# Kernel tuning notes

Hardware: AMD Instinct MI355X
Metric: run time of the kernel (lower is better)

Reference implementation:

```python
import jax, jax.numpy as jnp
import numpy as np

B, L, D, H, DH, MAX_SEQ = 2, 2048, 512, 8, 64, 2048


def setup_inputs() -> dict:
    key = jax.random.key(0)
    ks = jax.random.split(key, 9)
    w = 0.02
    return {
        "q": jax.random.normal(ks[0], (B, L, D), jnp.float32),
        "k": jax.random.normal(ks[1], (B, L, D), jnp.float32),
        "v": jax.random.normal(ks[2], (B, L, D), jnp.float32),
        "Wq_w": jax.random.normal(ks[3], (D, D), jnp.float32) * w,
        "Wq_b": jnp.zeros((D,), jnp.float32),
        "Wk_w": jax.random.normal(ks[4], (D, D), jnp.float32) * w,
        "Wk_b": jnp.zeros((D,), jnp.float32),
        "Wv_w": jax.random.normal(ks[5], (D, D), jnp.float32) * w,
        "Wv_b": jnp.zeros((D,), jnp.float32),
        "fc_w": jax.random.normal(ks[6], (D, D), jnp.float32) * w,
        "fc_b": jnp.zeros((D,), jnp.float32),
        "E": jax.random.normal(ks[7], (MAX_SEQ, DH), jnp.float32),
        "mask": jnp.triu(jnp.ones((L, L), jnp.int32), k=1)[None, None],  # 1 = masked
    }


def reference(q, k, v, Wq_w, Wq_b, Wk_w, Wk_b, Wv_w, Wv_b, fc_w, fc_b, E, mask):
    b, lq, d = q.shape

    def proj(x, w, bias):
        # torch Linear: x @ W.T + b, then split heads -> [b, h, l, dh]
        y = x @ w.T + bias
        return y.reshape(b, -1, H, DH).transpose(0, 2, 1, 3)

    qh, kh, vh = proj(q, Wq_w, Wq_b), proj(k, Wk_w, Wk_b), proj(v, Wv_w, Wv_b)
    len_q, len_k = qh.shape[2], kh.shape[2]

    # relative embedding slice (starting_point = max(0, max_seq - len_q))
    e = E[max(0, MAX_SEQ - len_q):, :]          # [m, dh], m == len_q here
    m = e.shape[0]

    QE = jnp.einsum('bhld,md->bhlm', qh, e)      # [b,h,lq,m]
    # qe_masking: keep column j of row i iff j >= m-1-i
    keep = (jnp.arange(m)[None, :] >= (m - 1 - jnp.arange(len_q))[:, None])
    QE = QE * keep.astype(QE.dtype)

    # skewing: left-pad last dim, reshape swapping trailing dims, drop first row
    padded = jnp.pad(QE, ((0, 0), (0, 0), (0, 0), (1, 0)))      # [b,h,lq,m+1]
    Srel = padded.reshape(b, H, m + 1, len_q)[:, :, 1:, :]       # [b,h,m,lq]
    if len_k > len_q:
        Srel = jnp.pad(Srel, ((0, 0), (0, 0), (0, len_k - len_q), (0, 0)))
    elif len_k < len_q:
        Srel = Srel[:, :, :, :len_k]

    QKt = jnp.einsum('bhld,bhmd->bhlm', qh, kh)                  # [b,h,lq,lk]
    logits = (QKt + Srel) / jnp.sqrt(jnp.float32(DH))
    logits = logits + mask.astype(logits.dtype) * jnp.float32(-1e9)
    attn = jax.nn.softmax(logits, axis=-1)
    out = jnp.einsum('bhlm,bhmd->bhld', attn, vh)                # [b,h,lq,dh]
    out = out.transpose(0, 2, 1, 3).reshape(b, len_q, d)
    out = out @ fc_w.T + fc_b
    return out, attn
```

## Files before the change

### kernel.cpp

```cpp
#include <hip/hip_runtime.h>
#include <hip/hip_bf16.h>
#include <cstdint>

typedef __bf16 bf16;
typedef __attribute__((ext_vector_type(8))) __bf16 bf16x8;
typedef __attribute__((ext_vector_type(4))) __bf16 bf16x4;
typedef __attribute__((ext_vector_type(4))) float f32x4;

#define MFMA16 __builtin_amdgcn_mfma_f32_16x16x32_bf16
#define MASKV (-1e30f)

static constexpr int Lq  = 2048;
static constexpr int BQ  = 64;
static constexpr int BKt = 64;
static constexpr int TW  = 84;

__device__ __forceinline__ void async_load16(const void* g, void* l) {
  __builtin_amdgcn_global_load_lds(
      (__attribute__((address_space(1))) void*)g,
      (__attribute__((address_space(3))) void*)l, 16, 0, 0);
}

__global__ void convert_all(const float* __restrict__ q, const float* __restrict__ k,
                            const float* __restrict__ v, const float* __restrict__ wq,
                            const float* __restrict__ wk, const float* __restrict__ wv,
                            const float* __restrict__ fc, const float* __restrict__ E,
                            bf16* q_bf, bf16* k_bf, bf16* v_bf, bf16* wq_bf,
                            bf16* wk_bf, bf16* wv_bf, bf16* fc_bf, bf16* E_bf)
{
  int i = blockIdx.x * blockDim.x + threadIdx.x;
  const float* src; bf16* dst; int rel;
  if      (i < 524288)  { src = q;  dst = q_bf;  rel = i; }
  else if (i < 1048576) { src = k;  dst = k_bf;  rel = i - 524288; }
  else if (i < 1572864) { src = v;  dst = v_bf;  rel = i - 1048576; }
  else if (i < 1638400) { src = wq; dst = wq_bf; rel = i - 1572864; }
  else if (i < 1703936) { src = wk; dst = wk_bf; rel = i - 1638400; }
  else if (i < 1769472) { src = wv; dst = wv_bf; rel = i - 1703936; }
  else if (i < 1835008) { src = fc; dst = fc_bf; rel = i - 1769472; }
  else if (i < 1867776) { src = E;  dst = E_bf;  rel = i - 1835008; }
  else return;
  float4 x = *(const float4*)(src + (size_t)rel * 4);
  bf16x4 o;
  o[0] = (bf16)x.x; o[1] = (bf16)x.y; o[2] = (bf16)x.z; o[3] = (bf16)x.w;
  *(bf16x4*)(dst + (size_t)rel * 4) = o;
}

__global__ void zero_s(float* __restrict__ s_buf) {
  int i = blockIdx.x * blockDim.x + threadIdx.x;
  if (i < 8192) ((float4*)s_buf)[i] = make_float4(0.f, 0.f, 0.f, 0.f);
}

__global__ void combine_o(const bf16* __restrict__ O0, const bf16* __restrict__ O1,
                          bf16* __restrict__ oh) {
  int i = blockIdx.x * blockDim.x + threadIdx.x;
  if (i >= 262144) return;
  bf16x8 a = *(const bf16x8*)(O0 + (size_t)i * 8);
  bf16x8 b = *(const bf16x8*)(O1 + (size_t)i * 8);
  bf16x8 o;
#pragma unroll
  for (int j = 0; j < 8; ++j) o[j] = (bf16)((float)a[j] + (float)b[j]);
  *(bf16x8*)(oh + (size_t)i * 8) = o;
}

template<int MODE>
__global__ __launch_bounds__(256, 2)
void gemm512(const bf16* __restrict__ A, const bf16* __restrict__ Bm,
             const float* __restrict__ bias, void* __restrict__ Cv)
{
  __shared__ __align__(16) char lA[16384];
  __shared__ __align__(16) char lB[16384];
  const int tid = threadIdx.x, lane = tid & 63, wv = tid >> 6;
  const int wr = wv >> 1, wc = wv & 1;
  const int tm = blockIdx.x, tn = blockIdx.y;

  f32x4 acc[4][4];
#pragma unroll
  for (int m = 0; m < 4; ++m)
#pragma unroll
    for (int n = 0; n < 4; ++n) acc[m][n] = (f32x4){0.f, 0.f, 0.f, 0.f};

  for (int k0 = 0; k0 < 512; k0 += 64) {
    __syncthreads();
#pragma unroll
    for (int it = 0; it < 4; ++it) {
      int slot = it * 256 + wv * 64 + lane;
      int row = slot >> 3, c = slot & 7;
      int gk = k0 + ((c ^ (row & 7)) * 8);
      async_load16(A  + (size_t)(tm * 128 + row) * 512 + gk, lA + (it * 256 + wv * 64) * 16);
      async_load16(Bm + (size_t)(tn * 128 + row) * 512 + gk, lB + (it * 256 + wv * 64) * 16);
    }
    __syncthreads();
#pragma unroll
    for (int kc = 0; kc < 2; ++kc) {
      bf16x8 af[4], bfr[4];
#pragma unroll
      for (int m = 0; m < 4; ++m) {
        int row = wr * 64 + m * 16 + (lane & 15);
        int ch = ((lane >> 4) + kc * 4) ^ (row & 7);
        af[m] = *(const bf16x8*)(lA + row * 128 + ch * 16);
      }
#pragma unroll
      for (int n = 0; n < 4; ++n) {
        int row = wc * 64 + n * 16 + (lane & 15);
        int ch = ((lane >> 4) + kc * 4) ^ (row & 7);
        bfr[n] = *(const bf16x8*)(lB + row * 128 + ch * 16);
      }
#pragma unroll
      for (int m = 0; m < 4; ++m)
#pragma unroll
        for (int n = 0; n < 4; ++n)
          acc[m][n] = MFMA16(af[m], bfr[n], acc[m][n], 0, 0, 0);
    }
  }

#pragma unroll
  for (int m = 0; m < 4; ++m)
#pragma unroll
    for (int n = 0; n < 4; ++n)
#pragma unroll
      for (int r = 0; r < 4; ++r) {
        int gi = tm * 128 + wr * 64 + m * 16 + 4 * (lane >> 4) + r;
        int gj = tn * 128 + wc * 64 + n * 16 + (lane & 15);
        float vv = acc[m][n][r] + ((MODE == 2) ? bias[gi] : bias[gj]);
        if (MODE == 3) {
          ((float*)Cv)[(size_t)gi * 512 + gj] = vv;
        } else if (MODE == 2) {
          int h = gi >> 6, dh = gi & 63, b = gj >> 11, l = gj & 2047;
          ((bf16*)Cv)[((size_t)((b * 8 + h) * 64 + dh)) * 2048 + l] = (bf16)vv;
        } else {
          int b = gi >> 11, l = gi & 2047, h = gj >> 6, dh = gj & 63;
          ((bf16*)Cv)[((size_t)((b * 8 + h) * 2048 + l)) * 64 + dh] = (bf16)vv;
        }
      }
}

__device__ __forceinline__ void stage_k(const bf16* __restrict__ kb, int j0,
                                        char* dst, int tid) {
#pragma unroll
  for (int it = 0; it < 2; ++it) {
    int slot = it * 256 + tid;
    int row = slot >> 3, c = slot & 7;
    async_load16(kb + (size_t)(j0 + row) * 64 + ((c ^ (row & 7)) * 8), dst + slot * 16);
  }
}
__device__ __forceinline__ void stage_v(const bf16* __restrict__ vb, int j0,
                                        char* dst, int tid) {
#pragma unroll
  for (int it = 0; it < 2; ++it) {
    int slot = it * 256 + tid;
    int row = slot >> 3, c = slot & 7;
    async_load16(vb + (size_t)row * Lq + j0 + ((c ^ (row & 7)) * 8), dst + slot * 16);
  }
}

__device__ __forceinline__ void attn_logits3(
    int i0, int j0, int wvx, int lane,
    const bf16x8 qf0, const bf16x8 qf1,
    const bf16* __restrict__ Ebf, const char* lk, bf16* tst, f32x4 acc_s[4])
{
  const int rbase = i0 + wvx * 16 - j0 - 63;
  f32x4 acc_t[5];
#pragma unroll
  for (int cf = 0; cf < 5; ++cf) {
    int r = rbase + cf * 16 + (lane & 15);
    int re = 2047 - r; re = re < 0 ? 0 : (re > 2047 ? 2047 : re);
    const bf16* ep = Ebf + (size_t)re * 64 + (lane >> 4) * 8;
    f32x4 a = (f32x4){0.f, 0.f, 0.f, 0.f};
    a = MFMA16(qf0, *(const bf16x8*)ep, a, 0, 0, 0);
    a = MFMA16(qf1, *(const bf16x8*)(ep + 32), a, 0, 0, 0);
    acc_t[cf] = a;
  }
#pragma unroll
  for (int cf = 0; cf < 4; ++cf) {
    int key = cf * 16 + (lane & 15);
    int c0 = (lane >> 4) ^ (key & 7);
    int c1 = ((lane >> 4) + 4) ^ (key & 7);
    f32x4 a = (f32x4){0.f, 0.f, 0.f, 0.f};
    a = MFMA16(qf0, *(const bf16x8*)(lk + key * 128 + c0 * 16), a, 0, 0, 0);
    a = MFMA16(qf1, *(const bf16x8*)(lk + key * 128 + c1 * 16), a, 0, 0, 0);
    acc_s[cf] = a;
  }
#pragma unroll
  for (int cf = 0; cf < 5; ++cf)
#pragma unroll
    for (int r = 0; r < 4; ++r)
      tst[(4 * (lane >> 4) + r) * TW + cf * 16 + (lane & 15)] = (bf16)acc_t[cf][r];
  asm volatile("s_waitcnt lgkmcnt(0)" ::: "memory");
  __builtin_amdgcn_sched_barrier(0);
#pragma unroll
  for (int cf = 0; cf < 4; ++cf) {
    int kl = cf * 16 + (lane & 15);
#pragma unroll
    for (int r = 0; r < 4; ++r) {
      int qw = 4 * (lane >> 4) + r;
      float t = (float)tst[qw * TW + (qw - kl + 63)];
      float vv = (acc_s[cf][r] + t) * 0.125f;
      if (j0 + kl > i0 + wvx * 16 + qw) vv = MASKV;
      acc_s[cf][r] = vv;
    }
  }
}

__global__ __launch_bounds__(256, 4)
void pass1_sums(const bf16* __restrict__ qh, const bf16* __restrict__ kh,
                const bf16* __restrict__ Ebf, float* __restrict__ s_buf)
{
  __shared__ __align__(16) char lds_k[2][64 * 128];
  __shared__ __align__(16) char lds_t[4][16 * TW * 2];
  const int tid = threadIdx.x, lane = tid & 63, wvx = tid >> 6;
  const int bid = blockIdx.x;
  const int bh  = bid / 144;
  int f = bid - bh * 144, qt = 0;
#pragma unroll 1
  for (int q = 0; q < 32; ++q) {
    int c = (q + 4) >> 2;
    if (f < c) { qt = q; break; }
    f -= c;
  }
  const int jbeg = f * 4;
  const int jend = (jbeg + 4 < qt + 1) ? jbeg + 4 : qt + 1;
  const int i0 = qt * BQ;

  const bf16* qb = qh + (size_t)bh * Lq * 64;
  const bf16* kb = kh + (size_t)bh * Lq * 64;
  bf16* tst = (bf16*)lds_t[wvx];

  const int qrow = i0 + wvx * 16 + (lane & 15);
  const bf16x8 qf0 = *(const bf16x8*)(qb + (size_t)qrow * 64 + (lane >> 4) * 8);
  const bf16x8 qf1 = *(const bf16x8*)(qb + (size_t)qrow * 64 + 32 + (lane >> 4) * 8);

  f32x4 acc_s[4];
  float s_acc[4] = {0.f, 0.f, 0.f, 0.f};

  stage_k(kb, jbeg * BKt, lds_k[0], tid);
  __syncthreads();
  for (int jt = jbeg; jt < jend; ++jt) {
    const int lt = (jt - jbeg) & 1;
    if (jt + 1 < jend) stage_k(kb, (jt + 1) * BKt, lds_k[lt ^ 1], tid);
    attn_logits3(i0, jt * BKt, wvx, lane, qf0, qf1, Ebf, lds_k[lt], tst, acc_s);
#pragma unroll
    for (int r = 0; r < 4; ++r) {
#pragma unroll
      for (int cf = 0; cf < 4; ++cf) s_acc[r] += __expf(acc_s[cf][r]);
    }
    __syncthreads();
  }
#pragma unroll
  for (int r = 0; r < 4; ++r) {
    float s = s_acc[r];
    for (int d = 1; d < 16; d <<= 1) s += __shfl_xor(s, d);
    if ((lane & 15) == 0)
      atomicAdd(&s_buf[bh * Lq + i0 + wvx * 16 + 4 * (lane >> 4) + r], s);
  }
}

__global__ __launch_bounds__(256, 3)
void attn_main(const bf16* __restrict__ qh, const bf16* __restrict__ kh,
               const bf16* __restrict__ vt, const bf16* __restrict__ Ebf,
               const float* __restrict__ s_buf, float* __restrict__ attn_out,
               bf16* __restrict__ O0, bf16* __restrict__ O1)
{
  __shared__ __align__(16) char lds_k[2][64 * 128];
  __shared__ __align__(16) char lds_v[2][64 * 128];
  __shared__ __align__(16) char lds_t[4][16 * TW * 2];

  const int tid = threadIdx.x, lane = tid & 63, wvx = tid >> 6;
  const int x    = blockIdx.x, jh = blockIdx.y;
  const int half = x >> 8;
  const int r0   = x & 255;
  const int xcd  = r0 & 7;
  const int idx  = r0 >> 3;
  const int bh   = 2 * xcd + half;
  const int qt   = half ? idx : 31 - idx;
  const int i0   = qt * BQ;
  const int njt  = qt + 1;
  const int nj0  = (njt + 1) >> 1;
  const int jbeg = jh ? nj0 : 0;
  const int jend = jh ? njt : nj0;
  bf16* Opart = jh ? O1 : O0;

  const bf16* qb = qh + (size_t)bh * Lq * 64;
  const bf16* kb = kh + (size_t)bh * Lq * 64;
  const bf16* vb = vt + (size_t)bh * 64 * Lq;
  float* attn_b = attn_out + (size_t)bh * Lq * Lq;
  bf16* tst = (bf16*)lds_t[wvx];
  bf16* pst = tst;

  const int qrow = i0 + wvx * 16 + (lane & 15);
  const bf16x8 qf0 = *(const bf16x8*)(qb + (size_t)qrow * 64 + (lane >> 4) * 8);
  const bf16x8 qf1 = *(const bf16x8*)(qb + (size_t)qrow * 64 + 32 + (lane >> 4) * 8);

  float inv_s[4];
#pragma unroll
  for (int r = 0; r < 4; ++r)
    inv_s[r] = 1.f / s_buf[bh * Lq + i0 + wvx * 16 + 4 * (lane >> 4) + r];

  f32x4 acc_s[4];
  f32x4 acc_o[4];
#pragma unroll
  for (int nn = 0; nn < 4; ++nn) acc_o[nn] = (f32x4){0.f, 0.f, 0.f, 0.f};

  if (jbeg < jend) {
    stage_k(kb, jbeg * BKt, lds_k[0], tid);
    stage_v(vb, jbeg * BKt, lds_v[0], tid);
    __syncthreads();
    for (int jt = jbeg; jt < jend; ++jt) {
      const int j0 = jt * BKt;
      const int lt = (jt - jbeg) & 1;
      if (jt + 1 < jend) {
        stage_k(kb, j0 + BKt, lds_k[lt ^ 1], tid);
        stage_v(vb, j0 + BKt, lds_v[lt ^ 1], tid);
      }
      attn_logits3(i0, j0, wvx, lane, qf0, qf1, Ebf, lds_k[lt], tst, acc_s);
      asm volatile("" ::: "memory");
#pragma unroll
      for (int cf = 0; cf < 4; ++cf) {
        int kl = cf * 16 + (lane & 15);
        int chs = kl >> 3;
#pragma unroll
        for (int r = 0; r < 4; ++r) {
          int qw = 4 * (lane >> 4) + r;
          float p = __expf(acc_s[cf][r]) * inv_s[r];
          pst[qw * 64 + ((chs ^ (qw & 7)) * 8) + (kl & 7)] = (bf16)p;
        }
      }
      asm volatile("s_waitcnt lgkmcnt(0)" ::: "memory");
      __builtin_amdgcn_sched_barrier(0);
#pragma unroll
      for (int it = 0; it < 2; ++it) {
        int qw = it * 8 + (lane >> 3);
        int c = lane & 7;
        bf16x8 pv = *(const bf16x8*)(pst + qw * 64 + ((c ^ (qw & 7)) * 8));
        float* dst = attn_b + (size_t)(i0 + wvx * 16 + qw) * Lq + j0 + c * 8;
        float4 f0, f1;
        f0.x = (float)pv[0]; f0.y = (float)pv[1]; f0.z = (float)pv[2]; f0.w = (float)pv[3];
        f1.x = (float)pv[4]; f1.y = (float)pv[5]; f1.z = (float)pv[6]; f1.w = (float)pv[7];
        *(float4*)dst = f0; *(float4*)(dst + 4) = f1;
      }
#pragma unroll
      for (int kc = 0; kc < 2; ++kc) {
        int qa = lane & 15;
        int cha = (kc * 4 + (lane >> 4)) ^ (qa & 7);
        bf16x8 pf = *(const bf16x8*)(pst + qa * 64 + cha * 8);
#pragma unroll
        for (int nn = 0; nn < 4; ++nn) {
          int dh = nn * 16 + (lane & 15);
          int chv = (kc * 4 + (lane >> 4)) ^ (dh & 7);
          bf16x8 vf = *(const bf16x8*)(lds_v[lt] + dh * 128 + chv * 16);
          acc_o[nn] = MFMA16(pf, vf, acc_o[nn], 0, 0, 0);
        }
      }
      __syncthreads();
    }
  }

  const int b = bh >> 3, h = bh & 7;
#pragma unroll
  for (int nn = 0; nn < 4; ++nn)
#pragma unroll
    for (int r = 0; r < 4; ++r) {
      int qw = 4 * (lane >> 4) + r;
      int ig = i0 + wvx * 16 + qw;
      int col = h * 64 + nn * 16 + (lane & 15);
      Opart[(size_t)(b * 2048 + ig) * 512 + col] = (bf16)acc_o[nn][r];
    }

  if (jh == 1) {
    const int jlane = (lane & 15) * 4;
    for (int j = njt * BKt + jlane; j < Lq; j += 64) {
#pragma unroll
      for (int r = 0; r < 4; ++r) {
        float* p = attn_b + (size_t)(i0 + wvx * 16 + 4 * (lane >> 4) + r) * Lq + j;
        *(float4*)p = make_float4(0.f, 0.f, 0.f, 0.f);
      }
    }
  }
}

extern "C" void kernel_launch(void* const* d_in, const int* in_sizes, int n_in,
                              void* d_out, int out_size, void* d_ws, size_t ws_size,
                              hipStream_t stream) {
  const float* q    = (const float*)d_in[0];
  const float* k    = (const float*)d_in[1];
  const float* v    = (const float*)d_in[2];
  const float* wq   = (const float*)d_in[3];
  const float* wq_b = (const float*)d_in[4];
  const float* wk   = (const float*)d_in[5];
  const float* wk_b = (const float*)d_in[6];
  const float* wv   = (const float*)d_in[7];
  const float* wv_b = (const float*)d_in[8];
  const float* fc   = (const float*)d_in[9];
  const float* fc_b = (const float*)d_in[10];
  const float* E    = (const float*)d_in[11];

  if (ws_size < 31719424) return;
  char* ws = (char*)d_ws;
  bf16* q_bf  = (bf16*)(ws);
  bf16* k_bf  = (bf16*)(ws + 4194304);
  bf16* v_bf  = (bf16*)(ws + 8388608);
  bf16* wq_bf = (bf16*)(ws + 12582912);
  bf16* wk_bf = (bf16*)(ws + 13107200);
  bf16* wv_bf = (bf16*)(ws + 13631488);
  bf16* fc_bf = (bf16*)(ws + 14155776);
  bf16* E_bf  = (bf16*)(ws + 14680064);
  bf16* qh_bf = (bf16*)(ws + 14942208);
  bf16* kh_bf = (bf16*)(ws + 19136512);
  bf16* vt_bf = (bf16*)(ws + 23330816);
  bf16* oh_bf = (bf16*)(ws + 27525120);

  bf16*  O0    = (bf16*)(ws);
  bf16*  O1    = (bf16*)(ws + 4194304);
  float* s_buf = (float*)(ws + 12582912);

  float* out_f  = (float*)d_out;
  float* attn_f = out_f + 2097152;

  convert_all<<<7296, 256, 0, stream>>>(q, k, v, wq, wk, wv, fc, E,
      q_bf, k_bf, v_bf, wq_bf, wk_bf, wv_bf, fc_bf, E_bf);
  gemm512<0><<<dim3(32, 4), 256, 0, stream>>>(q_bf, wq_bf, wq_b, qh_bf);
  zero_s<<<32, 256, 0, stream>>>(s_buf);
  gemm512<0><<<dim3(32, 4), 256, 0, stream>>>(k_bf, wk_bf, wk_b, kh_bf);
  gemm512<2><<<dim3(4, 32), 256, 0, stream>>>(wv_bf, v_bf, wv_b, vt_bf);
  pass1_sums<<<2304, 256, 0, stream>>>(qh_bf, kh_bf, E_bf, s_buf);
  attn_main<<<dim3(512, 2), 256, 0, stream>>>(qh_bf, kh_bf, vt_bf, E_bf,
                                              s_buf, attn_f, O0, O1);
  combine_o<<<1024, 256, 0, stream>>>(O0, O1, oh_bf);
  gemm512<3><<<dim3(32, 4), 256, 0, stream>>>(oh_bf, fc_bf, fc_b, out_f);
}
```

Baseline: 213.0 us.

## Split attention into fixed 4-tile key chunks, shuffle-based skew, fp32 slot reduction

The main attention kernel now gives each block one query tile and a fixed chunk of up to four key tiles, instead of two halves per query row. Partial outputs go to fp32 per-chunk slots, and a rewritten combine kernel sums them. The relative-position skew now uses cross-lane shuffles instead of an LDS staging buffer, which frees LDS and allows higher occupancy bounds in both pass1 and attn_main. Fully masked chunks only write zeros to the attention output. The cost is a much larger workspace and extra fp32 partial-output traffic.

```diff
diff --git a/kernel.cpp b/kernel.cpp
--- a/kernel.cpp
+++ b/kernel.cpp
@@ -11,9 +11,7 @@
 #define MASKV (-1e30f)
 
 static constexpr int Lq  = 2048;
-static constexpr int BQ  = 64;
 static constexpr int BKt = 64;
-static constexpr int TW  = 84;
 
 __device__ __forceinline__ void async_load16(const void* g, void* l) {
   __builtin_amdgcn_global_load_lds(
@@ -50,18 +48,6 @@
   if (i < 8192) ((float4*)s_buf)[i] = make_float4(0.f, 0.f, 0.f, 0.f);
 }
 
-__global__ void combine_o(const bf16* __restrict__ O0, const bf16* __restrict__ O1,
-                          bf16* __restrict__ oh) {
-  int i = blockIdx.x * blockDim.x + threadIdx.x;
-  if (i >= 262144) return;
-  bf16x8 a = *(const bf16x8*)(O0 + (size_t)i * 8);
-  bf16x8 b = *(const bf16x8*)(O1 + (size_t)i * 8);
-  bf16x8 o;
-#pragma unroll
-  for (int j = 0; j < 8; ++j) o[j] = (bf16)((float)a[j] + (float)b[j]);
-  *(bf16x8*)(oh + (size_t)i * 8) = o;
-}
-
 template<int MODE>
 __global__ __launch_bounds__(256, 2)
 void gemm512(const bf16* __restrict__ A, const bf16* __restrict__ Bm,
@@ -153,10 +139,10 @@
   }
 }
 
-__device__ __forceinline__ void attn_logits3(
+__device__ __forceinline__ void attn_logits_sh(
     int i0, int j0, int wvx, int lane,
     const bf16x8 qf0, const bf16x8 qf1,
-    const bf16* __restrict__ Ebf, const char* lk, bf16* tst, f32x4 acc_s[4])
+    const bf16* __restrict__ Ebf, const char* lk, f32x4 acc_s[4])
 {
   const int rbase = i0 + wvx * 16 - j0 - 63;
   f32x4 acc_t[5];
@@ -180,50 +166,47 @@
     a = MFMA16(qf1, *(const bf16x8*)(lk + key * 128 + c1 * 16), a, 0, 0, 0);
     acc_s[cf] = a;
   }
-#pragma unroll
-  for (int cf = 0; cf < 5; ++cf)
-#pragma unroll
-    for (int r = 0; r < 4; ++r)
-      tst[(4 * (lane >> 4) + r) * TW + cf * 16 + (lane & 15)] = (bf16)acc_t[cf][r];
-  asm volatile("s_waitcnt lgkmcnt(0)" ::: "memory");
-  __builtin_amdgcn_sched_barrier(0);
-#pragma unroll
-  for (int cf = 0; cf < 4; ++cf) {
-    int kl = cf * 16 + (lane & 15);
-#pragma unroll
-    for (int r = 0; r < 4; ++r) {
-      int qw = 4 * (lane >> 4) + r;
-      float t = (float)tst[qw * TW + (qw - kl + 63)];
+  const int g = lane >> 4, b = lane & 15;
+#pragma unroll
+  for (int r = 0; r < 4; ++r) {
+    const int qw  = 4 * g + r;
+    const int sl  = (lane & 48) | ((63 + qw - b) & 15);
+    const bool hi = qw > b;
+#pragma unroll
+    for (int cf = 0; cf < 4; ++cf) {
+      float vhi = __shfl(acc_t[4 - cf][r], sl);
+      float vlo = __shfl(acc_t[3 - cf][r], sl);
+      float t = hi ? vhi : vlo;
       float vv = (acc_s[cf][r] + t) * 0.125f;
-      if (j0 + kl > i0 + wvx * 16 + qw) vv = MASKV;
+      if (j0 + cf * 16 + b > i0 + wvx * 16 + qw) vv = MASKV;
       acc_s[cf][r] = vv;
     }
   }
 }
 
-__global__ __launch_bounds__(256, 4)
+__global__ __launch_bounds__(256, 5)
 void pass1_sums(const bf16* __restrict__ qh, const bf16* __restrict__ kh,
                 const bf16* __restrict__ Ebf, float* __restrict__ s_buf)
 {
   __shared__ __align__(16) char lds_k[2][64 * 128];
-  __shared__ __align__(16) char lds_t[4][16 * TW * 2];
   const int tid = threadIdx.x, lane = tid & 63, wvx = tid >> 6;
-  const int bid = blockIdx.x;
-  const int bh  = bid / 144;
-  int f = bid - bh * 144, qt = 0;
+  const int n    = blockIdx.x;
+  const int xcd  = n & 7;
+  const int r0   = n >> 3;
+  const int bh   = 2 * xcd + (r0 & 1);
+  int rem = r0 >> 1, qt = 31, f = 0;
 #pragma unroll 1
-  for (int q = 0; q < 32; ++q) {
-    int c = (q + 4) >> 2;
-    if (f < c) { qt = q; break; }
-    f -= c;
+  for (int q = 31; q >= 0; --q) {
+    int c = (q >> 2) + 1;
+    if (rem < c) { qt = q; f = rem; break; }
+    rem -= c;
   }
   const int jbeg = f * 4;
   const int jend = (jbeg + 4 < qt + 1) ? jbeg + 4 : qt + 1;
-  const int i0 = qt * BQ;
+  const int i0 = qt * 64;
 
   const bf16* qb = qh + (size_t)bh * Lq * 64;
   const bf16* kb = kh + (size_t)bh * Lq * 64;
-  bf16* tst = (bf16*)lds_t[wvx];
 
   const int qrow = i0 + wvx * 16 + (lane & 15);
   const bf16x8 qf0 = *(const bf16x8*)(qb + (size_t)qrow * 64 + (lane >> 4) * 8);
@@ -237,7 +220,7 @@
   for (int jt = jbeg; jt < jend; ++jt) {
     const int lt = (jt - jbeg) & 1;
     if (jt + 1 < jend) stage_k(kb, (jt + 1) * BKt, lds_k[lt ^ 1], tid);
-    attn_logits3(i0, jt * BKt, wvx, lane, qf0, qf1, Ebf, lds_k[lt], tst, acc_s);
+    attn_logits_sh(i0, jt * BKt, wvx, lane, qf0, qf1, Ebf, lds_k[lt], acc_s);
 #pragma unroll
     for (int r = 0; r < 4; ++r) {
 #pragma unroll
@@ -254,53 +237,50 @@
   }
 }
 
-__global__ __launch_bounds__(256, 3)
+__global__ __launch_bounds__(256, 4)
 void attn_main(const bf16* __restrict__ qh, const bf16* __restrict__ kh,
                const bf16* __restrict__ vt, const bf16* __restrict__ Ebf,
                const float* __restrict__ s_buf, float* __restrict__ attn_out,
-               bf16* __restrict__ O0, bf16* __restrict__ O1)
+               float* __restrict__ O_slots)
 {
   __shared__ __align__(16) char lds_k[2][64 * 128];
   __shared__ __align__(16) char lds_v[2][64 * 128];
-  __shared__ __align__(16) char lds_t[4][16 * TW * 2];
+  __shared__ __align__(16) char lds_p[4][16 * 64 * 2];
 
   const int tid = threadIdx.x, lane = tid & 63, wvx = tid >> 6;
-  const int x    = blockIdx.x, jh = blockIdx.y;
-  const int half = x >> 8;
-  const int r0   = x & 255;
-  const int xcd  = r0 & 7;
-  const int idx  = r0 >> 3;
-  const int bh   = 2 * xcd + half;
-  const int qt   = half ? idx : 31 - idx;
-  const int i0   = qt * BQ;
-  const int njt  = qt + 1;
-  const int nj0  = (njt + 1) >> 1;
-  const int jbeg = jh ? nj0 : 0;
-  const int jend = jh ? njt : nj0;
-  bf16* Opart = jh ? O1 : O0;
-
-  const bf16* qb = qh + (size_t)bh * Lq * 64;
-  const bf16* kb = kh + (size_t)bh * Lq * 64;
-  const bf16* vb = vt + (size_t)bh * 64 * Lq;
+  const int n    = blockIdx.x;
+  const int xcd  = n & 7;
+  const int r0   = n >> 3;
+  const int bh   = 2 * xcd + (r0 & 1);
+  const int u    = r0 >> 1;
+  const int f    = u >> 5;
+  const int qt   = u & 31;
+  const int i0   = qt * 64;
+  const int jbeg = f * 4;
+  const int jend = (jbeg + 4 < qt + 1) ? jbeg + 4 : qt + 1;
+
   float* attn_b = attn_out + (size_t)bh * Lq * Lq;
-  bf16* tst = (bf16*)lds_t[wvx];
-  bf16* pst = tst;
-
-  const int qrow = i0 + wvx * 16 + (lane & 15);
-  const bf16x8 qf0 = *(const bf16x8*)(qb + (size_t)qrow * 64 + (lane >> 4) * 8);
-  const bf16x8 qf1 = *(const bf16x8*)(qb + (size_t)qrow * 64 + 32 + (lane >> 4) * 8);
-
-  float inv_s[4];
-#pragma unroll
-  for (int r = 0; r < 4; ++r)
-    inv_s[r] = 1.f / s_buf[bh * Lq + i0 + wvx * 16 + 4 * (lane >> 4) + r];
-
-  f32x4 acc_s[4];
-  f32x4 acc_o[4];
-#pragma unroll
-  for (int nn = 0; nn < 4; ++nn) acc_o[nn] = (f32x4){0.f, 0.f, 0.f, 0.f};
-
-  if (jbeg < jend) {
+
+  if (jbeg <= qt) {
+    const bf16* qb = qh + (size_t)bh * Lq * 64;
+    const bf16* kb = kh + (size_t)bh * Lq * 64;
+    const bf16* vb = vt + (size_t)bh * 64 * Lq;
+    bf16* pst = (bf16*)lds_p[wvx];
+
+    const int qrow = i0 + wvx * 16 + (lane & 15);
+    const bf16x8 qf0 = *(const bf16x8*)(qb + (size_t)qrow * 64 + (lane >> 4) * 8);
+    const bf16x8 qf1 = *(const bf16x8*)(qb + (size_t)qrow * 64 + 32 + (lane >> 4) * 8);
+
+    float inv_s[4];
+#pragma unroll
+    for (int r = 0; r < 4; ++r)
+      inv_s[r] = 1.f / s_buf[bh * Lq + i0 + wvx * 16 + 4 * (lane >> 4) + r];
+
+    f32x4 acc_s[4];
+    f32x4 acc_o[4];
+#pragma unroll
+    for (int nn = 0; nn < 4; ++nn) acc_o[nn] = (f32x4){0.f, 0.f, 0.f, 0.f};
+
     stage_k(kb, jbeg * BKt, lds_k[0], tid);
     stage_v(vb, jbeg * BKt, lds_v[0], tid);
     __syncthreads();
@@ -311,8 +291,7 @@
         stage_k(kb, j0 + BKt, lds_k[lt ^ 1], tid);
         stage_v(vb, j0 + BKt, lds_v[lt ^ 1], tid);
       }
-      attn_logits3(i0, j0, wvx, lane, qf0, qf1, Ebf, lds_k[lt], tst, acc_s);
-      asm volatile("" ::: "memory");
+      attn_logits_sh(i0, j0, wvx, lane, qf0, qf1, Ebf, lds_k[lt], acc_s);
 #pragma unroll
       for (int cf = 0; cf < 4; ++cf) {
         int kl = cf * 16 + (lane & 15);
@@ -352,28 +331,48 @@
       }
       __syncthreads();
     }
-  }
-
+
+    float* oslot = O_slots + (size_t)(((bh * 32 + qt) * 8 + f)) * 4096;
+#pragma unroll
+    for (int nn = 0; nn < 4; ++nn)
+#pragma unroll
+      for (int r = 0; r < 4; ++r) {
+        int row = wvx * 16 + 4 * (lane >> 4) + r;
+        oslot[row * 64 + nn * 16 + (lane & 15)] = acc_o[nn][r];
+      }
+  }
+
+  for (int jt = (jbeg > qt + 1 ? jbeg : qt + 1); jt < jbeg + 4; ++jt) {
+    const int j0 = jt * BKt;
+#pragma unroll
+    for (int kk = 0; kk < 4; ++kk) {
+      int idx = kk * 256 + tid;
+      int row = idx >> 4, c4 = idx & 15;
+      float* p = attn_b + (size_t)(i0 + row) * Lq + j0 + c4 * 4;
+      *(float4*)p = make_float4(0.f, 0.f, 0.f, 0.f);
+    }
+  }
+}
+
+__global__ void combine_o(const float* __restrict__ O_slots, bf16* __restrict__ oh)
+{
+  const int sid = blockIdx.x;
+  const int bh = sid >> 5, qt = sid & 31;
+  const int nch = (qt >> 2) + 1;
+  const float* base = O_slots + (size_t)(bh * 32 + qt) * 8 * 4096;
   const int b = bh >> 3, h = bh & 7;
-#pragma unroll
-  for (int nn = 0; nn < 4; ++nn)
-#pragma unroll
-    for (int r = 0; r < 4; ++r) {
-      int qw = 4 * (lane >> 4) + r;
-      int ig = i0 + wvx * 16 + qw;
-      int col = h * 64 + nn * 16 + (lane & 15);
-      Opart[(size_t)(b * 2048 + ig) * 512 + col] = (bf16)acc_o[nn][r];
-    }
-
-  if (jh == 1) {
-    const int jlane = (lane & 15) * 4;
-    for (int j = njt * BKt + jlane; j < Lq; j += 64) {
-#pragma unroll
-      for (int r = 0; r < 4; ++r) {
-        float* p = attn_b + (size_t)(i0 + wvx * 16 + 4 * (lane >> 4) + r) * Lq + j;
-        *(float4*)p = make_float4(0.f, 0.f, 0.f, 0.f);
-      }
-    }
+  for (int e4 = threadIdx.x; e4 < 1024; e4 += 256) {
+    float4 s = make_float4(0.f, 0.f, 0.f, 0.f);
+    for (int ff = 0; ff < nch; ++ff) {
+      float4 x = *(const float4*)(base + ff * 4096 + e4 * 4);
+      s.x += x.x; s.y += x.y; s.z += x.z; s.w += x.w;
+    }
+    int row = (e4 * 4) >> 6;
+    int col = (e4 * 4) & 63;
+    int ig = qt * 64 + row;
+    bf16x4 o;
+    o[0] = (bf16)s.x; o[1] = (bf16)s.y; o[2] = (bf16)s.z; o[3] = (bf16)s.w;
+    *(bf16x4*)(oh + (size_t)(b * 2048 + ig) * 512 + h * 64 + col) = o;
   }
 }
 
@@ -393,37 +392,35 @@
   const float* fc_b = (const float*)d_in[10];
   const float* E    = (const float*)d_in[11];
 
-  if (ws_size < 31719424) return;
+  if (ws_size < 98959360) return;
   char* ws = (char*)d_ws;
-  bf16* q_bf  = (bf16*)(ws);
-  bf16* k_bf  = (bf16*)(ws + 4194304);
-  bf16* v_bf  = (bf16*)(ws + 8388608);
-  bf16* wq_bf = (bf16*)(ws + 12582912);
-  bf16* wk_bf = (bf16*)(ws + 13107200);
-  bf16* wv_bf = (bf16*)(ws + 13631488);
-  bf16* fc_bf = (bf16*)(ws + 14155776);
-  bf16* E_bf  = (bf16*)(ws + 14680064);
-  bf16* qh_bf = (bf16*)(ws + 14942208);
-  bf16* kh_bf = (bf16*)(ws + 19136512);
-  bf16* vt_bf = (bf16*)(ws + 23330816);
-  bf16* oh_bf = (bf16*)(ws + 27525120);
-
-  bf16*  O0    = (bf16*)(ws);
-  bf16*  O1    = (bf16*)(ws + 4194304);
-  float* s_buf = (float*)(ws + 12582912);
+  bf16*  q_bf    = (bf16*)(ws);
+  bf16*  k_bf    = (bf16*)(ws + 4194304);
+  bf16*  v_bf    = (bf16*)(ws + 8388608);
+  bf16*  wq_bf   = (bf16*)(ws + 12582912);
+  bf16*  wk_bf   = (bf16*)(ws + 13107200);
+  bf16*  wv_bf   = (bf16*)(ws + 13631488);
+  bf16*  fc_bf   = (bf16*)(ws + 14155776);
+  bf16*  E_bf    = (bf16*)(ws + 14680064);
+  float* s_buf   = (float*)(ws + 14942208);
+  bf16*  qh_bf   = (bf16*)(ws + 15073280);
+  bf16*  kh_bf   = (bf16*)(ws + 19267584);
+  bf16*  vt_bf   = (bf16*)(ws + 23461888);
+  bf16*  oh_bf   = (bf16*)(ws + 27656192);
+  float* O_slots = (float*)(ws + 31850496);
 
   float* out_f  = (float*)d_out;
   float* attn_f = out_f + 2097152;
 
   convert_all<<<7296, 256, 0, stream>>>(q, k, v, wq, wk, wv, fc, E,
       q_bf, k_bf, v_bf, wq_bf, wk_bf, wv_bf, fc_bf, E_bf);
+  zero_s<<<32, 256, 0, stream>>>(s_buf);
   gemm512<0><<<dim3(32, 4), 256, 0, stream>>>(q_bf, wq_bf, wq_b, qh_bf);
-  zero_s<<<32, 256, 0, stream>>>(s_buf);
   gemm512<0><<<dim3(32, 4), 256, 0, stream>>>(k_bf, wk_bf, wk_b, kh_bf);
   gemm512<2><<<dim3(4, 32), 256, 0, stream>>>(wv_bf, v_bf, wv_b, vt_bf);
   pass1_sums<<<2304, 256, 0, stream>>>(qh_bf, kh_bf, E_bf, s_buf);
-  attn_main<<<dim3(512, 2), 256, 0, stream>>>(qh_bf, kh_bf, vt_bf, E_bf,
-                                              s_buf, attn_f, O0, O1);
-  combine_o<<<1024, 256, 0, stream>>>(O0, O1, oh_bf);
+  attn_main<<<4096, 256, 0, stream>>>(qh_bf, kh_bf, vt_bf, E_bf,
+                                      s_buf, attn_f, O_slots);
+  combine_o<<<512, 256, 0, stream>>>(O_slots, oh_bf);
   gemm512<3><<<dim3(32, 4), 256, 0, stream>>>(oh_bf, fc_bf, fc_b, out_f);
 }
```

Result: slower. 221.3 us (+3.9%).
